# Performance work log

Hardware: AMD Instinct MI355X
Metric: run time of the kernel (lower is better)

Reference implementation:

```python
import jax, jax.numpy as jnp
import numpy as np

B, L, S, H, C = 64, 512, 512, 768, 9  # batch, bert subword len, word seq len, hidden, num_classes


def setup_inputs() -> dict:
    key = jax.random.key(0)
    k1, k2, k3 = jax.random.split(key, 3)
    rng = np.random.RandomState(0)
    # per-word subword counts in {1,2,3}; truncate so totals fit in L subword slots
    lens = rng.randint(1, 4, size=(B, S))
    cum = lens.cumsum(axis=1)
    keep = cum <= L
    ids_lens = (lens * keep).astype(np.int32)
    totals = ids_lens.sum(axis=1)
    attention_mask = (np.arange(L)[None, :] < totals[:, None]).astype(np.int32)
    label_mask = ids_lens > 0
    label_ids = (rng.randint(0, C, size=(B, S)) * label_mask).astype(np.int32)
    bert_out = jax.random.normal(k1, (B, L, H), dtype=jnp.float32)
    W = jax.random.normal(k2, (H, C), dtype=jnp.float32) * 0.02
    b = jnp.zeros((C,), dtype=jnp.float32)
    return {
        "bert_out": bert_out,
        "W": W,
        "b": b,
        "attention_mask": jnp.asarray(attention_mask),
        "ids_lens": jnp.asarray(ids_lens),
        "label_ids": jnp.asarray(label_ids),
        "label_mask": jnp.asarray(label_mask),
    }


def reference(bert_out, W, b, attention_mask, ids_lens, label_ids, label_mask):
    Bv, Lv, Hv = bert_out.shape
    Sv = ids_lens.shape[1]
    nseg = Bv * Sv
    am = attention_mask.astype(jnp.int32)
    # subword position within each example's valid region
    sidx = jnp.cumsum(am, axis=1) - 1                       # [B, L]
    # word index for each subword: searchsorted into cumulative word lengths
    ends = jnp.cumsum(ids_lens, axis=1)                     # [B, S]
    widx = jax.vmap(lambda e, s: jnp.searchsorted(e, s, side='right'))(ends, sidx)
    seg = jnp.where(am > 0, widx + jnp.arange(Bv)[:, None] * Sv, nseg)  # pad bucket = nseg
    flat = bert_out.reshape(Bv * Lv, Hv)
    segf = seg.reshape(Bv * Lv)
    sums = jax.ops.segment_sum(flat, segf, num_segments=nseg + 1)[:nseg]
    cnts = jax.ops.segment_sum(jnp.ones((Bv * Lv,), bert_out.dtype), segf,
                               num_segments=nseg + 1)[:nseg]
    mean = sums / jnp.maximum(cnts, 1.0)[:, None]           # segment mean (split().mean(0))
    word_mask = (ids_lens > 0).reshape(nseg)
    embed = jnp.where(word_mask[:, None], mean, 0.0).reshape(Bv, Sv, Hv)  # masked_scatter
    # dropout in eval mode = identity
    logits = embed @ W + b                                  # [B, S, C]
    logp = jax.nn.log_softmax(logits, axis=-1)
    lab = jnp.clip(label_ids, 0, W.shape[1] - 1)
    nll = -jnp.take_along_axis(logp, lab[..., None].astype(jnp.int32), axis=-1)[..., 0]
    valid = label_mask.astype(bert_out.dtype)
    loss = jnp.sum(nll * valid) / jnp.maximum(jnp.sum(valid), 1.0)
    pred = jnp.argmax(logits, axis=-1)
    return loss, pred
```

## Files before the change

### kernel.cpp

```cpp
#include <hip/hip_runtime.h>
#include <math.h>

#define BB 64
#define LL 512
#define SS 512
#define HH 768
#define CC 9
#define WPB 32
#define GF (BB * SS / WPB)
#define NPART (GF * 4)

template <int CTRL>
__device__ __forceinline__ float dpp_add(float x) {
    int y = __builtin_amdgcn_update_dpp(0, __float_as_int(x), CTRL, 0xf, 0xf, true);
    return x + __int_as_float(y);
}
__device__ __forceinline__ float rsum64(float x) {
    x = dpp_add<0x111>(x);
    x = dpp_add<0x112>(x);
    x = dpp_add<0x114>(x);
    x = dpp_add<0x118>(x);
    x = dpp_add<0x142>(x);
    x = dpp_add<0x143>(x);
    return x;
}

__global__ __launch_bounds__(256) void wt_kernel(const float* __restrict__ Wm,
                                                 float* __restrict__ WT_g) {
    int e = blockIdx.x * 256 + threadIdx.x;
    if (e < HH * CC) {
        int h = e / CC;
        int c = e - h * CC;
        WT_g[c * HH + h] = Wm[e];
    }
}

__global__ __launch_bounds__(256) void fused_kernel(
    const float* __restrict__ bert,
    const float* __restrict__ WT_g,
    const float* __restrict__ bias,
    const int* __restrict__ ids_lens,
    const int* __restrict__ label_ids,
    float* __restrict__ pred_out,
    float* __restrict__ nll_part,
    float* __restrict__ cnt_part)
{
    __shared__ int wlen[WPB];
    __shared__ int woff[WPB + 1];
    __shared__ float red[4];
    __shared__ int s_start_sh;

    int b = blockIdx.x >> 4;
    int chunk = blockIdx.x & 15;
    int w0 = chunk * WPB;
    const int* lens = ids_lens + b * SS;
    int t = threadIdx.x, lane = t & 63, wave = t >> 6;

    if (t < WPB) wlen[t] = lens[w0 + t];

    int part = 0;
    for (int i = t; i < w0; i += 256) part += lens[i];
    float pf = rsum64((float)part);
    if (lane == 63) red[wave] = pf;
    __syncthreads();
    if (t == 0) {
        int run = 0;
#pragma unroll
        for (int k = 0; k < WPB; k++) { woff[k] = run; run += wlen[k]; }
        woff[WPB] = run;
        s_start_sh = (int)(red[0] + red[1] + red[2] + red[3]);
    }
    __syncthreads();

    int hoff = lane * 4;
    float4 wreg[CC][3];
#pragma unroll
    for (int c = 0; c < CC; c++)
#pragma unroll
        for (int c3 = 0; c3 < 3; c3++)
            wreg[c][c3] = *reinterpret_cast<const float4*>(WT_g + c * HH + c3 * 256 + hoff);

    float bs[CC];
#pragma unroll
    for (int c = 0; c < CC; c++) bs[c] = bias[c];

    int w8 = wave * 8;
    int row0 = s_start_sh + woff[w8];
    int nrows = woff[w8 + 8] - woff[w8];
    const float* p = bert + ((size_t)b * LL + row0) * HH + hoff;

    float4 n0, n1, n2;
    n0.x = n0.y = n0.z = n0.w = 0.0f; n1 = n0; n2 = n0;
    if (nrows > 0) {
        n0 = *reinterpret_cast<const float4*>(p);
        n1 = *reinterpret_cast<const float4*>(p + 256);
        n2 = *reinterpret_cast<const float4*>(p + 512);
    }
    int j = 0;
    float nll_acc = 0.0f, cnt_acc = 0.0f;

    for (int k = 0; k < 8; ++k) {
        int len = wlen[w8 + k];
        float acc[CC];
#pragma unroll
        for (int c = 0; c < CC; c++) acc[c] = 0.0f;

        for (int jj = 0; jj < len; ++jj) {
#pragma unroll
            for (int c = 0; c < CC; c++) {
                acc[c] += n0.x * wreg[c][0].x + n0.y * wreg[c][0].y
                        + n0.z * wreg[c][0].z + n0.w * wreg[c][0].w
                        + n1.x * wreg[c][1].x + n1.y * wreg[c][1].y
                        + n1.z * wreg[c][1].z + n1.w * wreg[c][1].w
                        + n2.x * wreg[c][2].x + n2.y * wreg[c][2].y
                        + n2.z * wreg[c][2].z + n2.w * wreg[c][2].w;
            }
            ++j;
            if (j < nrows) {
                const float* q = p + (size_t)j * HH;
                n0 = *reinterpret_cast<const float4*>(q);
                n1 = *reinterpret_cast<const float4*>(q + 256);
                n2 = *reinterpret_cast<const float4*>(q + 512);
            }
        }

#pragma unroll
        for (int c = 0; c < CC; c++) acc[c] = rsum64(acc[c]);

        if (lane == 63) {
            float inv = 1.0f / (float)(len > 0 ? len : 1);
            float lg[CC];
#pragma unroll
            for (int c = 0; c < CC; c++) lg[c] = acc[c] * inv + bs[c];

            float mx = lg[0];
            int arg = 0;
#pragma unroll
            for (int c = 1; c < CC; c++) {
                if (lg[c] > mx) { mx = lg[c]; arg = c; }
            }
            float se = 0.0f;
#pragma unroll
            for (int c = 0; c < CC; c++) se += expf(lg[c] - mx);
            float lse = mx + logf(se);

            int g = b * SS + w0 + w8 + k;
            int lab = label_ids[g];
            lab = lab < 0 ? 0 : (lab > CC - 1 ? CC - 1 : lab);
            float valid = (len > 0) ? 1.0f : 0.0f;
            pred_out[g] = (float)arg;
            nll_acc += (lse - lg[lab]) * valid;
            cnt_acc += valid;
        }
    }

    if (lane == 63) {
        int pid = blockIdx.x * 4 + wave;
        nll_part[pid] = nll_acc;
        cnt_part[pid] = cnt_acc;
    }
}

__global__ __launch_bounds__(1024) void finalize_kernel(
    const float* __restrict__ nll_part,
    const float* __restrict__ cnt_part,
    float* __restrict__ out_loss) {
    __shared__ float sn[16], sc[16];
    int t = threadIdx.x, lane = t & 63, wave = t >> 6;
    float n = 0.0f, c = 0.0f;
#pragma unroll
    for (int i = 0; i < NPART / 1024; ++i) {
        n += nll_part[t + i * 1024];
        c += cnt_part[t + i * 1024];
    }
    n = rsum64(n);
    c = rsum64(c);
    if (lane == 63) { sn[wave] = n; sc[wave] = c; }
    __syncthreads();
    if (t == 0) {
        float tn = 0.0f, tc = 0.0f;
#pragma unroll
        for (int i = 0; i < 16; i++) { tn += sn[i]; tc += sc[i]; }
        out_loss[0] = tn / fmaxf(tc, 1.0f);
    }
}

extern "C" void kernel_launch(void* const* d_in, const int* in_sizes, int n_in,
                              void* d_out, int out_size, void* d_ws, size_t ws_size,
                              hipStream_t stream) {
    const float* bert = (const float*)d_in[0];
    const float* Wm   = (const float*)d_in[1];
    const float* bias = (const float*)d_in[2];
    const int* ids_lens  = (const int*)d_in[4];
    const int* label_ids = (const int*)d_in[5];

    float* out = (float*)d_out;

    float* WT_g     = (float*)d_ws;
    float* nll_part = WT_g + CC * HH;
    float* cnt_part = nll_part + NPART;

    wt_kernel<<<(HH * CC + 255) / 256, 256, 0, stream>>>(Wm, WT_g);
    fused_kernel<<<GF, 256, 0, stream>>>(bert, WT_g, bias, ids_lens, label_ids,
                                         out + 1, nll_part, cnt_part);
    finalize_kernel<<<1, 1024, 0, stream>>>(nll_part, cnt_part, out);
}
```

Baseline: 187.7 us.

## Double-buffer per-word row loads, sum rows before dot, W in LDS

Halves words per block (16, four per wave) to double the grid and adds an occupancy hint to launch bounds. W is staged in shared memory instead of 108 registers. Each word's up to three subword rows are loaded at once and summed before one dot product per class, and loads for the next word overlap the current word's epilogue. Blocks with no valid words exit early. The risks are more LDS traffic per word, a fixed three-row limit per word, and a 27 KB LDS footprint per block.

```diff
diff --git a/kernel.cpp b/kernel.cpp
--- a/kernel.cpp
+++ b/kernel.cpp
@@ -6,7 +6,8 @@
 #define SS 512
 #define HH 768
 #define CC 9
-#define WPB 32
+#define WPW 4
+#define WPB 16
 #define GF (BB * SS / WPB)
 #define NPART (GF * 4)
 
@@ -25,6 +26,13 @@
     return x;
 }
 
+__device__ __forceinline__ float4 f4add(float4 a, float4 b) {
+    return make_float4(a.x + b.x, a.y + b.y, a.z + b.z, a.w + b.w);
+}
+__device__ __forceinline__ float dot4(float4 a, float4 b) {
+    return a.x * b.x + a.y * b.y + a.z * b.z + a.w * b.w;
+}
+
 __global__ __launch_bounds__(256) void wt_kernel(const float* __restrict__ Wm,
                                                  float* __restrict__ WT_g) {
     int e = blockIdx.x * 256 + threadIdx.x;
@@ -35,7 +43,7 @@
     }
 }
 
-__global__ __launch_bounds__(256) void fused_kernel(
+__global__ __launch_bounds__(256, 2) void fused_kernel(
     const float* __restrict__ bert,
     const float* __restrict__ WT_g,
     const float* __restrict__ bias,
@@ -45,13 +53,14 @@
     float* __restrict__ nll_part,
     float* __restrict__ cnt_part)
 {
+    __shared__ float wt_sh[CC * HH];
     __shared__ int wlen[WPB];
     __shared__ int woff[WPB + 1];
     __shared__ float red[4];
     __shared__ int s_start_sh;
 
-    int b = blockIdx.x >> 4;
-    int chunk = blockIdx.x & 15;
+    int b = blockIdx.x >> 5;
+    int chunk = blockIdx.x & 31;
     int w0 = chunk * WPB;
     const int* lens = ids_lens + b * SS;
     int t = threadIdx.x, lane = t & 63, wave = t >> 6;
@@ -72,92 +81,106 @@
     }
     __syncthreads();
 
+    int tot_rows = woff[WPB];
+    if (tot_rows == 0) {
+        if (t < WPB) {
+            float mx = bias[0]; int arg = 0;
+#pragma unroll
+            for (int c = 1; c < CC; c++) { float v = bias[c]; if (v > mx) { mx = v; arg = c; } }
+            pred_out[b * SS + w0 + t] = (float)arg;
+        }
+        if (t < 4) { nll_part[blockIdx.x * 4 + t] = 0.0f; cnt_part[blockIdx.x * 4 + t] = 0.0f; }
+        return;
+    }
+
+    {
+        const float4* src = reinterpret_cast<const float4*>(WT_g);
+        float4* dst = reinterpret_cast<float4*>(wt_sh);
+#pragma unroll
+        for (int i = 0; i < 7; i++) {
+            int idx = t + i * 256;
+            if (idx < (CC * HH / 4)) dst[idx] = src[idx];
+        }
+    }
+    __syncthreads();
+
+    float bsr[CC];
+#pragma unroll
+    for (int c = 0; c < CC; c++) bsr[c] = bias[c];
+
     int hoff = lane * 4;
-    float4 wreg[CC][3];
-#pragma unroll
-    for (int c = 0; c < CC; c++)
-#pragma unroll
-        for (int c3 = 0; c3 < 3; c3++)
-            wreg[c][c3] = *reinterpret_cast<const float4*>(WT_g + c * HH + c3 * 256 + hoff);
-
-    float bs[CC];
-#pragma unroll
-    for (int c = 0; c < CC; c++) bs[c] = bias[c];
-
-    int w8 = wave * 8;
-    int row0 = s_start_sh + woff[w8];
-    int nrows = woff[w8 + 8] - woff[w8];
-    const float* p = bert + ((size_t)b * LL + row0) * HH + hoff;
-
-    float4 n0, n1, n2;
-    n0.x = n0.y = n0.z = n0.w = 0.0f; n1 = n0; n2 = n0;
-    if (nrows > 0) {
-        n0 = *reinterpret_cast<const float4*>(p);
-        n1 = *reinterpret_cast<const float4*>(p + 256);
-        n2 = *reinterpret_cast<const float4*>(p + 512);
-    }
-    int j = 0;
+    int w8 = wave * WPW;
+    size_t rowbase = (size_t)b * LL + (size_t)s_start_sh;
     float nll_acc = 0.0f, cnt_acc = 0.0f;
 
-    for (int k = 0; k < 8; ++k) {
-        int len = wlen[w8 + k];
-        float acc[CC];
-#pragma unroll
-        for (int c = 0; c < CC; c++) acc[c] = 0.0f;
-
-        for (int jj = 0; jj < len; ++jj) {
-#pragma unroll
-            for (int c = 0; c < CC; c++) {
-                acc[c] += n0.x * wreg[c][0].x + n0.y * wreg[c][0].y
-                        + n0.z * wreg[c][0].z + n0.w * wreg[c][0].w
-                        + n1.x * wreg[c][1].x + n1.y * wreg[c][1].y
-                        + n1.z * wreg[c][1].z + n1.w * wreg[c][1].w
-                        + n2.x * wreg[c][2].x + n2.y * wreg[c][2].y
-                        + n2.z * wreg[c][2].z + n2.w * wreg[c][2].w;
-            }
-            ++j;
-            if (j < nrows) {
-                const float* q = p + (size_t)j * HH;
-                n0 = *reinterpret_cast<const float4*>(q);
-                n1 = *reinterpret_cast<const float4*>(q + 256);
-                n2 = *reinterpret_cast<const float4*>(q + 512);
-            }
-        }
-
-#pragma unroll
-        for (int c = 0; c < CC; c++) acc[c] = rsum64(acc[c]);
-
-        if (lane == 63) {
-            float inv = 1.0f / (float)(len > 0 ? len : 1);
-            float lg[CC];
-#pragma unroll
-            for (int c = 0; c < CC; c++) lg[c] = acc[c] * inv + bs[c];
-
-            float mx = lg[0];
-            int arg = 0;
-#pragma unroll
-            for (int c = 1; c < CC; c++) {
-                if (lg[c] > mx) { mx = lg[c]; arg = c; }
-            }
-            float se = 0.0f;
-#pragma unroll
-            for (int c = 0; c < CC; c++) se += expf(lg[c] - mx);
-            float lse = mx + logf(se);
-
-            int g = b * SS + w0 + w8 + k;
-            int lab = label_ids[g];
-            lab = lab < 0 ? 0 : (lab > CC - 1 ? CC - 1 : lab);
-            float valid = (len > 0) ? 1.0f : 0.0f;
-            pred_out[g] = (float)arg;
-            nll_acc += (lse - lg[lab]) * valid;
-            cnt_acc += valid;
-        }
-    }
+    float4 a00, a01, a02, a10, a11, a12, a20, a21, a22;
+    float4 b00, b01, b02, b10, b11, b12, b20, b21, b22;
+
+#define LDROW(pb_, r_, ch_) (*reinterpret_cast<const float4*>((pb_) + (size_t)(r_) * HH + (ch_) * 256))
+#define ISSUE(P0, P1, P2, P3, P4, P5, P6, P7, P8, KN) do {                         \
+    int ln_ = wlen[w8 + (KN)];                                                     \
+    const float* pb_ = bert + (rowbase + (size_t)woff[w8 + (KN)]) * HH + hoff;     \
+    if (ln_ > 0) { P0 = LDROW(pb_, 0, 0); P1 = LDROW(pb_, 0, 1); P2 = LDROW(pb_, 0, 2); } \
+    if (ln_ > 1) { P3 = LDROW(pb_, 1, 0); P4 = LDROW(pb_, 1, 1); P5 = LDROW(pb_, 1, 2); } \
+    if (ln_ > 2) { P6 = LDROW(pb_, 2, 0); P7 = LDROW(pb_, 2, 1); P8 = LDROW(pb_, 2, 2); } \
+} while (0)
+
+#define EPI(Q0, Q1, Q2, Q3, Q4, Q5, Q6, Q7, Q8, KN) do {                           \
+    int len_ = wlen[w8 + (KN)];                                                    \
+    float acc_[CC];                                                                \
+    if (len_ > 0) {                                                                \
+        float4 s0_ = Q0, s1_ = Q1, s2_ = Q2;                                       \
+        if (len_ > 1) { s0_ = f4add(s0_, Q3); s1_ = f4add(s1_, Q4); s2_ = f4add(s2_, Q5); } \
+        if (len_ > 2) { s0_ = f4add(s0_, Q6); s1_ = f4add(s1_, Q7); s2_ = f4add(s2_, Q8); } \
+        _Pragma("unroll")                                                          \
+        for (int c = 0; c < CC; c++) {                                             \
+            float4 w0_ = *reinterpret_cast<const float4*>(&wt_sh[c * HH + hoff]);         \
+            float4 w1_ = *reinterpret_cast<const float4*>(&wt_sh[c * HH + 256 + hoff]);   \
+            float4 w2_ = *reinterpret_cast<const float4*>(&wt_sh[c * HH + 512 + hoff]);   \
+            acc_[c] = dot4(s0_, w0_) + dot4(s1_, w1_) + dot4(s2_, w2_);            \
+        }                                                                          \
+        _Pragma("unroll")                                                          \
+        for (int c = 0; c < CC; c++) acc_[c] = rsum64(acc_[c]);                    \
+    } else {                                                                       \
+        _Pragma("unroll")                                                          \
+        for (int c = 0; c < CC; c++) acc_[c] = 0.0f;                               \
+    }                                                                              \
+    if (lane == 63) {                                                              \
+        float inv_ = (len_ > 0) ? (1.0f / (float)len_) : 1.0f;                     \
+        float lg_[CC];                                                             \
+        _Pragma("unroll")                                                          \
+        for (int c = 0; c < CC; c++) lg_[c] = acc_[c] * inv_ + bsr[c];             \
+        float mx_ = lg_[0]; int arg_ = 0;                                          \
+        _Pragma("unroll")                                                          \
+        for (int c = 1; c < CC; c++) { if (lg_[c] > mx_) { mx_ = lg_[c]; arg_ = c; } } \
+        float se_ = 0.0f;                                                          \
+        _Pragma("unroll")                                                          \
+        for (int c = 0; c < CC; c++) se_ += expf(lg_[c] - mx_);                    \
+        float lse_ = mx_ + logf(se_);                                              \
+        int g_ = b * SS + w0 + w8 + (KN);                                          \
+        int lab_ = label_ids[g_];                                                  \
+        lab_ = lab_ < 0 ? 0 : (lab_ > CC - 1 ? CC - 1 : lab_);                     \
+        if (len_ > 0) { nll_acc += lse_ - lg_[lab_]; cnt_acc += 1.0f; }            \
+        pred_out[g_] = (float)arg_;                                                \
+    }                                                                              \
+} while (0)
+
+    ISSUE(a00, a01, a02, a10, a11, a12, a20, a21, a22, 0);
+    ISSUE(b00, b01, b02, b10, b11, b12, b20, b21, b22, 1);
+    EPI(a00, a01, a02, a10, a11, a12, a20, a21, a22, 0);
+    ISSUE(a00, a01, a02, a10, a11, a12, a20, a21, a22, 2);
+    EPI(b00, b01, b02, b10, b11, b12, b20, b21, b22, 1);
+    ISSUE(b00, b01, b02, b10, b11, b12, b20, b21, b22, 3);
+    EPI(a00, a01, a02, a10, a11, a12, a20, a21, a22, 2);
+    EPI(b00, b01, b02, b10, b11, b12, b20, b21, b22, 3);
+
+#undef EPI
+#undef ISSUE
+#undef LDROW
 
     if (lane == 63) {
-        int pid = blockIdx.x * 4 + wave;
-        nll_part[pid] = nll_acc;
-        cnt_part[pid] = cnt_acc;
+        nll_part[blockIdx.x * 4 + wave] = nll_acc;
+        cnt_part[blockIdx.x * 4 + wave] = cnt_acc;
     }
 }
 
```

After: 200.1 us. +6.6%, slower.

## Precompute word offsets with a scan kernel and give each wave two words

Applied to the files above, without the earlier changes.

A separate kernel now computes per-word subword offsets with a wave-shuffle prefix scan, and its extra block does the W transpose. The main kernel gives each wave two words instead of eight. It loads all (at most three) subword rows for both words up front and sums them before doing a single dot product with W. This removes the serial per-block prefix sum and the dependent row-by-row load chain, exposing much more memory-level parallelism. The costs are many more blocks, W reloaded for every wave, and the assumption that a word never has more than three subwords.

```diff
diff --git a/kernel.cpp b/kernel.cpp
--- a/kernel.cpp
+++ b/kernel.cpp
@@ -6,9 +6,10 @@
 #define SS 512
 #define HH 768
 #define CC 9
-#define WPB 32
-#define GF (BB * SS / WPB)
-#define NPART (GF * 4)
+#define WPV 2
+#define WPB (WPV * 4)
+#define GW (BB * SS / WPB)
+#define NPART (GW * 4)
 
 template <int CTRL>
 __device__ __forceinline__ float dpp_add(float x) {
@@ -25,137 +26,155 @@
     return x;
 }
 
-__global__ __launch_bounds__(256) void wt_kernel(const float* __restrict__ Wm,
-                                                 float* __restrict__ WT_g) {
-    int e = blockIdx.x * 256 + threadIdx.x;
-    if (e < HH * CC) {
-        int h = e / CC;
-        int c = e - h * CC;
-        WT_g[c * HH + h] = Wm[e];
-    }
-}
-
-__global__ __launch_bounds__(256) void fused_kernel(
+__device__ __forceinline__ float4 f4add(float4 a, float4 b) {
+    return make_float4(a.x + b.x, a.y + b.y, a.z + b.z, a.w + b.w);
+}
+__device__ __forceinline__ float dot4(float4 a, float4 b) {
+    return a.x * b.x + a.y * b.y + a.z * b.z + a.w * b.w;
+}
+
+__global__ __launch_bounds__(512) void scan_wt_kernel(
+    const int* __restrict__ ids_lens,
+    const float* __restrict__ Wm,
+    int* __restrict__ woff_g,
+    float* __restrict__ WT_g)
+{
+    if (blockIdx.x == BB) {
+        for (int e = threadIdx.x; e < HH * CC; e += 512) {
+            int h = e / CC;
+            int c = e - h * CC;
+            WT_g[c * HH + h] = Wm[e];
+        }
+        return;
+    }
+    __shared__ int wtot[8];
+    int b = blockIdx.x;
+    int t = threadIdx.x, lane = t & 63, wave = t >> 6;
+    int len = ids_lens[b * SS + t];
+    int x = len;
+#pragma unroll
+    for (int off = 1; off < 64; off <<= 1) {
+        int y = __shfl_up(x, off);
+        if (lane >= off) x += y;
+    }
+    if (lane == 63) wtot[wave] = x;
+    __syncthreads();
+    int base = 0;
+    for (int wv = 0; wv < wave; wv++) base += wtot[wv];
+    woff_g[b * SS + t] = base + x - len;
+}
+
+__global__ __launch_bounds__(256, 4) void word_kernel(
     const float* __restrict__ bert,
     const float* __restrict__ WT_g,
     const float* __restrict__ bias,
     const int* __restrict__ ids_lens,
+    const int* __restrict__ woff_g,
     const int* __restrict__ label_ids,
     float* __restrict__ pred_out,
     float* __restrict__ nll_part,
     float* __restrict__ cnt_part)
 {
-    __shared__ int wlen[WPB];
-    __shared__ int woff[WPB + 1];
-    __shared__ float red[4];
-    __shared__ int s_start_sh;
-
-    int b = blockIdx.x >> 4;
-    int chunk = blockIdx.x & 15;
-    int w0 = chunk * WPB;
-    const int* lens = ids_lens + b * SS;
     int t = threadIdx.x, lane = t & 63, wave = t >> 6;
-
-    if (t < WPB) wlen[t] = lens[w0 + t];
-
-    int part = 0;
-    for (int i = t; i < w0; i += 256) part += lens[i];
-    float pf = rsum64((float)part);
-    if (lane == 63) red[wave] = pf;
-    __syncthreads();
-    if (t == 0) {
-        int run = 0;
-#pragma unroll
-        for (int k = 0; k < WPB; k++) { woff[k] = run; run += wlen[k]; }
-        woff[WPB] = run;
-        s_start_sh = (int)(red[0] + red[1] + red[2] + red[3]);
-    }
-    __syncthreads();
-
     int hoff = lane * 4;
-    float4 wreg[CC][3];
-#pragma unroll
-    for (int c = 0; c < CC; c++)
-#pragma unroll
-        for (int c3 = 0; c3 < 3; c3++)
-            wreg[c][c3] = *reinterpret_cast<const float4*>(WT_g + c * HH + c3 * 256 + hoff);
+    int gA = blockIdx.x * WPB + wave * WPV;
+    int gB = gA + 1;
+    int pid = blockIdx.x * 4 + wave;
+
+    int lenA = ids_lens[gA];
+    int lenB = ids_lens[gB];
 
     float bs[CC];
 #pragma unroll
     for (int c = 0; c < CC; c++) bs[c] = bias[c];
 
-    int w8 = wave * 8;
-    int row0 = s_start_sh + woff[w8];
-    int nrows = woff[w8 + 8] - woff[w8];
-    const float* p = bert + ((size_t)b * LL + row0) * HH + hoff;
-
-    float4 n0, n1, n2;
-    n0.x = n0.y = n0.z = n0.w = 0.0f; n1 = n0; n2 = n0;
-    if (nrows > 0) {
-        n0 = *reinterpret_cast<const float4*>(p);
-        n1 = *reinterpret_cast<const float4*>(p + 256);
-        n2 = *reinterpret_cast<const float4*>(p + 512);
-    }
-    int j = 0;
-    float nll_acc = 0.0f, cnt_acc = 0.0f;
-
-    for (int k = 0; k < 8; ++k) {
-        int len = wlen[w8 + k];
-        float acc[CC];
-#pragma unroll
-        for (int c = 0; c < CC; c++) acc[c] = 0.0f;
-
-        for (int jj = 0; jj < len; ++jj) {
-#pragma unroll
-            for (int c = 0; c < CC; c++) {
-                acc[c] += n0.x * wreg[c][0].x + n0.y * wreg[c][0].y
-                        + n0.z * wreg[c][0].z + n0.w * wreg[c][0].w
-                        + n1.x * wreg[c][1].x + n1.y * wreg[c][1].y
-                        + n1.z * wreg[c][1].z + n1.w * wreg[c][1].w
-                        + n2.x * wreg[c][2].x + n2.y * wreg[c][2].y
-                        + n2.z * wreg[c][2].z + n2.w * wreg[c][2].w;
-            }
-            ++j;
-            if (j < nrows) {
-                const float* q = p + (size_t)j * HH;
-                n0 = *reinterpret_cast<const float4*>(q);
-                n1 = *reinterpret_cast<const float4*>(q + 256);
-                n2 = *reinterpret_cast<const float4*>(q + 512);
-            }
+    if ((lenA | lenB) == 0) {
+        if (lane == 63) {
+            float mx = bs[0]; int arg = 0;
+#pragma unroll
+            for (int c = 1; c < CC; c++) { if (bs[c] > mx) { mx = bs[c]; arg = c; } }
+            pred_out[gA] = (float)arg;
+            pred_out[gB] = (float)arg;
+            nll_part[pid] = 0.0f;
+            cnt_part[pid] = 0.0f;
         }
-
-#pragma unroll
-        for (int c = 0; c < CC; c++) acc[c] = rsum64(acc[c]);
-
-        if (lane == 63) {
-            float inv = 1.0f / (float)(len > 0 ? len : 1);
+        return;
+    }
+
+    const float4 z4 = make_float4(0.f, 0.f, 0.f, 0.f);
+    float4 PA0 = z4, PA1 = z4, PA2 = z4;
+    float4 PB0 = z4, PB1 = z4, PB2 = z4;
+
+#define LD3(dst0, dst1, dst2, base_, r_)                                         \
+    do {                                                                         \
+        const float* q_ = (base_) + (size_t)(r_) * HH;                           \
+        dst0 = *reinterpret_cast<const float4*>(q_);                             \
+        dst1 = *reinterpret_cast<const float4*>(q_ + 256);                       \
+        dst2 = *reinterpret_cast<const float4*>(q_ + 512);                       \
+    } while (0)
+
+    {
+        int bA = gA >> 9;
+        const float* pA = bert + ((size_t)bA * LL + woff_g[gA]) * HH + hoff;
+        float4 r0a, r1a, r2a, r0b, r1b, r2b, r0c, r1c, r2c;
+        if (lenA > 0) LD3(r0a, r1a, r2a, pA, 0);
+        if (lenA > 1) LD3(r0b, r1b, r2b, pA, 1);
+        if (lenA > 2) LD3(r0c, r1c, r2c, pA, 2);
+        if (lenA > 0) { PA0 = r0a; PA1 = r1a; PA2 = r2a; }
+        if (lenA > 1) { PA0 = f4add(PA0, r0b); PA1 = f4add(PA1, r1b); PA2 = f4add(PA2, r2b); }
+        if (lenA > 2) { PA0 = f4add(PA0, r0c); PA1 = f4add(PA1, r1c); PA2 = f4add(PA2, r2c); }
+    }
+    {
+        int bB = gB >> 9;
+        const float* pB = bert + ((size_t)bB * LL + woff_g[gB]) * HH + hoff;
+        float4 r0a, r1a, r2a, r0b, r1b, r2b, r0c, r1c, r2c;
+        if (lenB > 0) LD3(r0a, r1a, r2a, pB, 0);
+        if (lenB > 1) LD3(r0b, r1b, r2b, pB, 1);
+        if (lenB > 2) LD3(r0c, r1c, r2c, pB, 2);
+        if (lenB > 0) { PB0 = r0a; PB1 = r1a; PB2 = r2a; }
+        if (lenB > 1) { PB0 = f4add(PB0, r0b); PB1 = f4add(PB1, r1b); PB2 = f4add(PB2, r2b); }
+        if (lenB > 2) { PB0 = f4add(PB0, r0c); PB1 = f4add(PB1, r1c); PB2 = f4add(PB2, r2c); }
+    }
+#undef LD3
+
+    float accA[CC], accB[CC];
+#pragma unroll
+    for (int c = 0; c < CC; c++) {
+        float4 w0 = *reinterpret_cast<const float4*>(WT_g + c * HH + hoff);
+        float4 w1 = *reinterpret_cast<const float4*>(WT_g + c * HH + 256 + hoff);
+        float4 w2 = *reinterpret_cast<const float4*>(WT_g + c * HH + 512 + hoff);
+        accA[c] = dot4(PA0, w0) + dot4(PA1, w1) + dot4(PA2, w2);
+        accB[c] = dot4(PB0, w0) + dot4(PB1, w1) + dot4(PB2, w2);
+    }
+#pragma unroll
+    for (int c = 0; c < CC; c++) {
+        accA[c] = rsum64(accA[c]);
+        accB[c] = rsum64(accB[c]);
+    }
+
+    if (lane == 63) {
+        float nll_acc = 0.0f, cnt_acc = 0.0f;
+#pragma unroll
+        for (int wsel = 0; wsel < 2; wsel++) {
+            int g = wsel ? gB : gA;
+            int len = wsel ? lenB : lenA;
+            float inv = (len > 0) ? (1.0f / (float)len) : 1.0f;
             float lg[CC];
 #pragma unroll
-            for (int c = 0; c < CC; c++) lg[c] = acc[c] * inv + bs[c];
-
-            float mx = lg[0];
-            int arg = 0;
-#pragma unroll
-            for (int c = 1; c < CC; c++) {
-                if (lg[c] > mx) { mx = lg[c]; arg = c; }
-            }
+            for (int c = 0; c < CC; c++)
+                lg[c] = (wsel ? accB[c] : accA[c]) * inv + bs[c];
+            float mx = lg[0]; int arg = 0;
+#pragma unroll
+            for (int c = 1; c < CC; c++) { if (lg[c] > mx) { mx = lg[c]; arg = c; } }
             float se = 0.0f;
 #pragma unroll
             for (int c = 0; c < CC; c++) se += expf(lg[c] - mx);
             float lse = mx + logf(se);
-
-            int g = b * SS + w0 + w8 + k;
             int lab = label_ids[g];
             lab = lab < 0 ? 0 : (lab > CC - 1 ? CC - 1 : lab);
-            float valid = (len > 0) ? 1.0f : 0.0f;
+            if (len > 0) { nll_acc += lse - lg[lab]; cnt_acc += 1.0f; }
             pred_out[g] = (float)arg;
-            nll_acc += (lse - lg[lab]) * valid;
-            cnt_acc += valid;
         }
-    }
-
-    if (lane == 63) {
-        int pid = blockIdx.x * 4 + wave;
         nll_part[pid] = nll_acc;
         cnt_part[pid] = cnt_acc;
     }
@@ -197,11 +216,12 @@
     float* out = (float*)d_out;
 
     float* WT_g     = (float*)d_ws;
-    float* nll_part = WT_g + CC * HH;
+    int*   woff_g   = (int*)(WT_g + CC * HH);
+    float* nll_part = (float*)(woff_g + BB * SS);
     float* cnt_part = nll_part + NPART;
 
-    wt_kernel<<<(HH * CC + 255) / 256, 256, 0, stream>>>(Wm, WT_g);
-    fused_kernel<<<GF, 256, 0, stream>>>(bert, WT_g, bias, ids_lens, label_ids,
-                                         out + 1, nll_part, cnt_part);
+    scan_wt_kernel<<<BB + 1, 512, 0, stream>>>(ids_lens, Wm, woff_g, WT_g);
+    word_kernel<<<GW, 256, 0, stream>>>(bert, WT_g, bias, ids_lens, woff_g,
+                                        label_ids, out + 1, nll_part, cnt_part);
     finalize_kernel<<<1, 1024, 0, stream>>>(nll_part, cnt_part, out);
 }
```

After: 179.7 us. 1.04x faster.
